# Kernel tuning notes

Hardware: AMD Instinct MI355X
Metric: run time of the kernel (lower is better)

## Reference

```python
import jax, jax.numpy as jnp
from jax import lax
import numpy as np

B, T, D, H = 64, 291, 300, 10
K = D // H  # 30
SLOPE = 0.01  # nn.LeakyReLU default
EPS = 1e-5


def _leaky(x):
    return jnp.where(x >= 0, x, SLOPE * x)


def _ln2d(x, g, b):
    # torch LayerNorm over the LAST TWO dims (normalized_shape=[t, d])
    mu = jnp.mean(x, axis=(-2, -1), keepdims=True)
    var = jnp.mean((x - mu) ** 2, axis=(-2, -1), keepdims=True)
    return (x - mu) / jnp.sqrt(var + EPS) * g + b


def _mha(x, Wq, Wk, Wv, Wm):
    # manual multi-head self-attention; q,k each scaled by h**-0.25
    b, t, d = x.shape
    s = H ** 0.25
    q = (x @ Wq.T).reshape(b, t, H, K) / s
    k = (x @ Wk.T).reshape(b, t, H, K) / s
    v = (x @ Wv.T).reshape(b, t, H, K)
    att = jax.nn.softmax(jnp.einsum('bihk,bjhk->bhij', q, k), axis=-1)
    o = jnp.einsum('bhij,bjhk->bihk', att, v).reshape(b, t, d)
    return o @ Wm.T


def _conv_head(R, W, b):
    # Conv2d(2,25,(kh,300)) valid -> [B,25,L,1]; leaky; global maxpool over L
    y = lax.conv_general_dilated(R, W, (1, 1), 'VALID',
                                 dimension_numbers=('NCHW', 'OIHW', 'NCHW'))
    y = _leaky(y + b[None, :, None, None])
    return jnp.max(y, axis=(2, 3))  # [B,25]


def setup_inputs() -> dict:
    key = jax.random.key(0)
    ks = jax.random.split(key, 32)
    it = iter(range(32))
    def n(shape, scale=0.05):
        return (jax.random.normal(ks[next(it)], shape, dtype=jnp.float32) * scale)
    inp = {
        'x1': jax.random.normal(ks[next(it)], (B, T, D), dtype=jnp.float32),
        'x2': jax.random.normal(ks[next(it)], (B, 1000), dtype=jnp.float32),
        'W_img': n((300, 1000)), 'b_img': jnp.zeros((300,), jnp.float32),
        'g1': jnp.ones((T, D), jnp.float32), 'be1': jnp.zeros((T, D), jnp.float32),
        'g2': jnp.ones((1, D), jnp.float32), 'be2': jnp.zeros((1, D), jnp.float32),
        'Wq_tp': n((D, D)), 'Wk_tp': n((D, D)), 'Wv_tp': n((D, D)),
        'Wq_pt': n((D, D)), 'Wk_pt': n((D, D)), 'Wv_pt': n((D, D)),
        'Wq1': n((D, D)), 'Wk1': n((D, D)), 'Wv1': n((D, D)), 'Wm1': n((D, D)),
        'Wq2': n((D, D)), 'Wk2': n((D, D)), 'Wv2': n((D, D)), 'Wm2': n((D, D)),
        'Wq3': n((D, D)), 'Wk3': n((D, D)), 'Wv3': n((D, D)), 'Wm3': n((D, D)),
        'Wc1': n((25, 2, 1, D)), 'Wc2': n((25, 2, 2, D)),
        'Wc3': n((25, 2, 3, D)), 'Wc4': n((25, 2, 4, D)),
        'bc1': jnp.zeros((25,), jnp.float32), 'bc2': jnp.zeros((25,), jnp.float32),
        'bc3': jnp.zeros((25,), jnp.float32), 'bc4': jnp.zeros((25,), jnp.float32),
        'Wlin': n((300, 100)), 'blin': jnp.zeros((300,), jnp.float32),
        'Wlast': n((2, 600)), 'blast': jnp.zeros((2,), jnp.float32),
    }
    return inp


def reference(x1, x2, W_img, b_img, g1, be1, g2, be2,
              Wq_tp, Wk_tp, Wv_tp, Wq_pt, Wk_pt, Wv_pt,
              Wq1, Wk1, Wv1, Wm1, Wq2, Wk2, Wv2, Wm2, Wq3, Wk3, Wv3, Wm3,
              Wc1, Wc2, Wc3, Wc4, bc1, bc2, bc3, bc4,
              Wlin, blin, Wlast, blast):
    # image branch: x2 is the frozen VGG19 1000-d encoding
    img = _leaky(x2 @ W_img.T + b_img)[:, None, :]      # [B,1,300]
    lnP = _ln2d(img, g2, be2)                           # [B,1,300]
    lnT = _ln2d(x1, g1, be1)                            # [B,291,300]

    # cross-attn T->P (query from image, kv from text), unscaled
    q = lnP @ Wq_tp.T; k = lnT @ Wk_tp.T; v = lnT @ Wv_tp.T
    a = jax.nn.softmax(jnp.einsum('bqd,btd->bqt', q, k), axis=-1)
    R_T_P = jnp.einsum('bqt,btd->bqd', a, v) + lnP      # [B,1,300]

    # cross-attn P->T (query from text, kv from image; softmax over size-1 dim)
    q = lnT @ Wq_pt.T; k = lnP @ Wk_pt.T; v = lnP @ Wv_pt.T
    a = jax.nn.softmax(jnp.einsum('btd,bqd->btq', q, k), axis=-1)
    R_P_T = jnp.einsum('btq,bqd->btd', a, v) + lnT      # [B,291,300]

    # 3 stacked multi-head self-attn blocks on the text stream
    a1 = _mha(lnT, Wq1, Wk1, Wv1, Wm1)
    a2 = _mha(a1, Wq2, Wk2, Wv2, Wm2)
    a3 = _mha(a2, Wq3, Wk3, Wv3, Wm3)

    R = jnp.stack((R_P_T, a3), axis=1)                  # [B,2,291,300]
    r1 = _conv_head(R, Wc1, bc1)
    r2 = _conv_head(R, Wc2, bc2)
    r3 = _conv_head(R, Wc3, bc3)
    r4 = _conv_head(R, Wc4, bc4)
    total = jnp.concatenate([r1, r2, r3, r4], axis=1)   # [B,100]
    total = _leaky(total @ Wlin.T + blin)               # [B,300]

    Y = jnp.concatenate([R_T_P[:, 0, :], total], axis=1) @ Wlast.T + blast
    return Y                                            # [B,2]
```

## Files before the change

kernel.cpp:

```cpp
#include <hip/hip_runtime.h>
#include <hip/hip_bf16.h>
#include <math.h>

#define Bn 64
#define Tn 291
#define Dn 300
#define Hn 10
#define Mn (Bn*Tn)
#define Mp 18688
#define Kp 320

typedef __bf16 bf16x8 __attribute__((ext_vector_type(8)));
typedef float f32x4 __attribute__((ext_vector_type(4)));

static __device__ __forceinline__ float leaky(float x){ return x >= 0.f ? x : 0.01f*x; }

template<int NT>
static __device__ __forceinline__ float blockSum(float v, float* red){
  __syncthreads();
  int lane = threadIdx.x & 63, wid = threadIdx.x >> 6;
  #pragma unroll
  for (int o = 32; o > 0; o >>= 1) v += __shfl_down(v, o, 64);
  if (lane == 0) red[wid] = v;
  __syncthreads();
  if (threadIdx.x == 0) {
    float s = red[0];
    #pragma unroll
    for (int w = 1; w < NT/64; ++w) s += red[w];
    red[0] = s;
  }
  __syncthreads();
  return red[0];
}

template<int NT>
static __device__ __forceinline__ float blockMax(float v, float* red){
  __syncthreads();
  int lane = threadIdx.x & 63, wid = threadIdx.x >> 6;
  #pragma unroll
  for (int o = 32; o > 0; o >>= 1) v = fmaxf(v, __shfl_down(v, o, 64));
  if (lane == 0) red[wid] = v;
  __syncthreads();
  if (threadIdx.x == 0) {
    float s = red[0];
    #pragma unroll
    for (int w = 1; w < NT/64; ++w) s = fmaxf(s, red[w]);
    red[0] = s;
  }
  __syncthreads();
  return red[0];
}

__global__ __launch_bounds__(256)
void k_img_lnp(const float* __restrict__ x2, const float* __restrict__ Wimg,
               const float* __restrict__ bimg, const float* __restrict__ g2,
               const float* __restrict__ be2, float* __restrict__ lnP)
{
  int b = blockIdx.x, tid = threadIdx.x;
  __shared__ float sx[1000];
  __shared__ float sy[300];
  __shared__ float red[4];
  for (int i = tid; i < 1000; i += 256) sx[i] = x2[b*1000 + i];
  __syncthreads();
  for (int j = tid; j < 300; j += 256) {
    const float* w = Wimg + j*1000;
    float a = 0.f;
    for (int i = 0; i < 1000; ++i) a += sx[i]*w[i];
    sy[j] = leaky(a + bimg[j]);
  }
  __syncthreads();
  float s = 0.f, ss = 0.f;
  for (int j = tid; j < 300; j += 256) { float v = sy[j]; s += v; ss += v*v; }
  float tot  = blockSum<256>(s, red);
  float tot2 = blockSum<256>(ss, red);
  float mu   = tot * (1.f/300.f);
  float var  = tot2 * (1.f/300.f) - mu*mu;
  float rstd = rsqrtf(var + 1e-5f);
  for (int j = tid; j < 300; j += 256)
    lnP[b*300 + j] = (sy[j]-mu)*rstd*g2[j] + be2[j];
}

__global__ __launch_bounds__(1024)
void k_lnT(const float* __restrict__ x1, const float* __restrict__ g1,
           const float* __restrict__ be1, float* __restrict__ outf,
           __hip_bfloat16* __restrict__ outb)
{
  int b = blockIdx.x, tid = threadIdx.x;
  __shared__ float red[16];
  const float4* xb = (const float4*)(x1 + (size_t)b*87300);
  const float4* g4 = (const float4*)g1;
  const float4* b4 = (const float4*)be1;
  float4* o4 = (float4*)(outf + (size_t)b*87300);
  float s = 0.f, ss = 0.f;
  for (int i = tid; i < 21825; i += 1024) {
    float4 v = xb[i];
    s  += v.x+v.y+v.z+v.w;
    ss += v.x*v.x+v.y*v.y+v.z*v.z+v.w*v.w;
  }
  float tot  = blockSum<1024>(s, red);
  float tot2 = blockSum<1024>(ss, red);
  float mu   = tot / 87300.f;
  float var  = tot2 / 87300.f - mu*mu;
  float rstd = rsqrtf(var + 1e-5f);
  for (int i = tid; i < 21825; i += 1024) {
    float4 v = xb[i], g = g4[i], be = b4[i], o;
    o.x = (v.x-mu)*rstd*g.x + be.x;
    o.y = (v.y-mu)*rstd*g.y + be.y;
    o.z = (v.z-mu)*rstd*g.z + be.z;
    o.w = (v.w-mu)*rstd*g.w + be.w;
    o4[i] = o;
  }
  const float* xs = x1 + (size_t)b*87300;
  for (int e = tid; e < Tn*Dn; e += 1024) {
    int t = e/300;
    float x = xs[e];
    outb[(size_t)(b*Tn+t)*Kp + (e - t*300)] = __float2bfloat16((x-mu)*rstd*g1[e] + be1[e]);
  }
  for (int e = tid; e < Tn*20; e += 1024) {
    int t = e/20, d = 300 + e%20;
    outb[(size_t)(b*Tn+t)*Kp + d] = __float2bfloat16(0.f);
  }
}

__global__ __launch_bounds__(320)
void k_tp(const float* __restrict__ lnP, const float* __restrict__ lnT,
          const float* __restrict__ Wq, const float* __restrict__ Wk,
          const float* __restrict__ Wv, const float* __restrict__ Wvpt,
          float* __restrict__ RTP, float* __restrict__ vpt)
{
  int b = blockIdx.x, tid = threadIdx.x;
  __shared__ float sP[300], sQ[300], sM[300], sA[291], sW[300], red[5];
  if (tid < 300) sP[tid] = lnP[b*300 + tid];
  __syncthreads();
  if (tid < 300) {
    const float* w = Wq + tid*300;
    float a = 0.f;
    for (int i = 0; i < 300; ++i) a += sP[i]*w[i];
    sQ[tid] = a;
  }
  __syncthreads();
  if (tid < 300) {
    float a = 0.f;
    for (int j = 0; j < 300; ++j) a += sQ[j]*Wk[j*300 + tid];
    sM[tid] = a;
  }
  __syncthreads();
  float sc = -1e30f;
  if (tid < 291) {
    const float* r = lnT + ((size_t)b*Tn + tid)*300;
    float a = 0.f;
    for (int i = 0; i < 300; ++i) a += r[i]*sM[i];
    sc = a;
  }
  float mx  = blockMax<320>(sc, red);
  float e   = (tid < 291) ? __expf(sc - mx) : 0.f;
  float den = blockSum<320>(e, red);
  if (tid < 291) sA[tid] = e;
  __syncthreads();
  if (tid < 300) {
    float a = 0.f;
    for (int t = 0; t < 291; ++t) a += sA[t]*lnT[((size_t)b*Tn + t)*300 + tid];
    sW[tid] = a / den;
  }
  __syncthreads();
  if (tid < 300) {
    const float* w = Wv + tid*300;
    float a = 0.f;
    for (int i = 0; i < 300; ++i) a += sW[i]*w[i];
    RTP[b*300 + tid] = a + sP[tid];
    const float* w2 = Wvpt + tid*300;
    float a2 = 0.f;
    for (int i = 0; i < 300; ++i) a2 += sP[i]*w2[i];
    vpt[b*300 + tid] = a2;
  }
}

__global__ __launch_bounds__(256)
void k_rptb(const float* __restrict__ lnT, const float* __restrict__ vpt,
            __hip_bfloat16* __restrict__ out)
{
  int idx = blockIdx.x*256 + threadIdx.x;
  if (idx >= Mn*Kp) return;
  int m = idx / Kp, d = idx - m*Kp;
  int b = m / Tn;
  float v = (d < 300) ? lnT[(size_t)m*300 + d] + vpt[b*300 + d] : 0.f;
  out[idx] = __float2bfloat16(v);
}

struct Wptrs { const float* p[12]; };
__global__ __launch_bounds__(256)
void k_wcvt(Wptrs wp, __hip_bfloat16* __restrict__ out)
{
  int idx = blockIdx.x*256 + threadIdx.x;
  if (idx >= 12*Kp*Kp) return;
  int mat = idx / (Kp*Kp);
  int rem = idx - mat*(Kp*Kp);
  int r = rem / Kp, c = rem - r*Kp;
  float v = (r < 300 && c < 300) ? wp.p[mat][r*300 + c] : 0.f;
  out[idx] = __float2bfloat16(v);
}

__global__ __launch_bounds__(256)
void k_wpackb(const float* __restrict__ Wc1, const float* __restrict__ Wc2,
              const float* __restrict__ Wc3, const float* __restrict__ Wc4,
              __hip_bfloat16* __restrict__ out)
{
  int idx = blockIdx.x*256 + threadIdx.x;
  if (idx >= 2*256*Kp) return;
  int c  = idx % Kp;
  int rc = idx / Kp;
  int ch = rc / 256;
  int r  = rc % 256;
  float v = 0.f;
  if (r < 250 && c < 300) {
    const float* W; int kh, ro;
    if      (r < 25)  { W = Wc1; kh = 1; ro = r;      }
    else if (r < 75)  { W = Wc2; kh = 2; ro = r - 25; }
    else if (r < 150) { W = Wc3; kh = 3; ro = r - 75; }
    else              { W = Wc4; kh = 4; ro = r - 150;}
    int o = ro/kh, dh = ro%kh;
    v = W[((o*2 + ch)*kh + dh)*300 + c];
  }
  out[idx] = __float2bfloat16(v);
}

__global__ __launch_bounds__(256)
void k_gemm3(const ushort* __restrict__ A0, const ushort* __restrict__ A1,
             const ushort* __restrict__ W0, const ushort* __restrict__ W1,
             ushort* __restrict__ C0, ushort* __restrict__ C1,
             int nn, int cpitch)
{
  const ushort* A = blockIdx.z ? A1 : A0;
  const ushort* W = blockIdx.z ? W1 : W0;
  ushort*       C = blockIdx.z ? C1 : C0;
  int total = gridDim.x;
  int bid = blockIdx.x;
  int q = total >> 3, r = total & 7;
  int xcd = bid & 7, idx = bid >> 3;
  int wgid = (xcd < r ? xcd*(q+1) : r*(q+1) + (xcd-r)*q) + idx;
  int m0 = (wgid / nn) * 128, n0 = (wgid % nn) * 64;

  __shared__ alignas(16) ushort As[2][128*64];
  __shared__ alignas(16) ushort Bs[2][64*64];
  int tid = threadIdx.x;
  int lane = tid & 63, w = tid >> 6, wr = w >> 1, wc = w & 1;
  int lm = lane & 15, lk = lane >> 4;
  f32x4 acc[4][2] = {};
  uint4 ra[4], rw[2];

  auto loadregs = [&](int kt){
    #pragma unroll
    for (int u = 0; u < 4; ++u) {
      int s = tid + u*256; int row = s >> 3, kg = s & 7;
      ra[u] = *(const uint4*)(A + (size_t)(m0+row)*Kp + kt*64 + kg*8);
    }
    #pragma unroll
    for (int u = 0; u < 2; ++u) {
      int s = tid + u*256; int row = s >> 3, kg = s & 7;
      rw[u] = *(const uint4*)(W + (size_t)(n0+row)*Kp + kt*64 + kg*8);
    }
  };
  auto writeLDS = [&](int buf){
    #pragma unroll
    for (int u = 0; u < 4; ++u) {
      int s = tid + u*256; int row = s >> 3, kg = s & 7;
      *(uint4*)&As[buf][row*64 + ((kg ^ (row&7)) << 3)] = ra[u];
    }
    #pragma unroll
    for (int u = 0; u < 2; ++u) {
      int s = tid + u*256; int row = s >> 3, kg = s & 7;
      *(uint4*)&Bs[buf][row*64 + ((kg ^ (row&7)) << 3)] = rw[u];
    }
  };
  auto compute = [&](int buf){
    #pragma unroll
    for (int s = 0; s < 2; ++s) {
      bf16x8 af[4], bfr[2];
      int kg = s*4 + lk;
      #pragma unroll
      for (int mf = 0; mf < 4; ++mf) {
        int rr = wr*64 + mf*16 + lm;
        af[mf] = *(const bf16x8*)&As[buf][rr*64 + ((kg ^ (rr&7)) << 3)];
      }
      #pragma unroll
      for (int nf = 0; nf < 2; ++nf) {
        int rr = wc*32 + nf*16 + lm;
        bfr[nf] = *(const bf16x8*)&Bs[buf][rr*64 + ((kg ^ (rr&7)) << 3)];
      }
      #pragma unroll
      for (int mf = 0; mf < 4; ++mf)
        #pragma unroll
        for (int nf = 0; nf < 2; ++nf)
          acc[mf][nf] = __builtin_amdgcn_mfma_f32_16x16x32_bf16(af[mf], bfr[nf], acc[mf][nf], 0, 0, 0);
    }
  };

  loadregs(0); writeLDS(0);
  __syncthreads();
  #pragma unroll 1
  for (int kt = 0; kt < 5; ++kt) {
    if (kt < 4) loadregs(kt+1);
    compute(kt & 1);
    if (kt < 4) {
      __syncthreads();
      writeLDS((kt+1) & 1);
      __syncthreads();
    }
  }
  __syncthreads();
  ushort* T = &As[0][0];
  #pragma unroll
  for (int mf = 0; mf < 4; ++mf)
    #pragma unroll
    for (int nf = 0; nf < 2; ++nf)
      #pragma unroll
      for (int i = 0; i < 4; ++i) {
        int rr = wr*64 + mf*16 + lk*4 + i;
        int cc = wc*32 + nf*16 + lm;
        __hip_bfloat16 t = __float2bfloat16(acc[mf][nf][i]);
        T[rr*72 + cc] = *(ushort*)&t;
      }
  __syncthreads();
  #pragma unroll
  for (int u = 0; u < 4; ++u) {
    int s = tid + u*256; int row = s >> 3, g = s & 7;
    uint4 v = *(const uint4*)&T[row*72 + g*8];
    *(uint4*)(C + (size_t)(m0+row)*cpitch + n0 + g*8) = v;
  }
}

__global__ __launch_bounds__(256)
void k_attn5(const ushort* __restrict__ X, ushort* __restrict__ O)
{
  int b = blockIdx.x, h = blockIdx.y, tid = threadIdx.x;
  __shared__ alignas(16) ushort Ks[320*40];
  __shared__ alignas(16) ushort Vt[32*328];
  __shared__ alignas(16) ushort Ps[64*168];
  const size_t rbase = (size_t)b*Tn*960;
  const int hq = h*30;
  for (int i = tid; i < 320*20; i += 256) {
    int r = i/20, c2 = i%20;
    uint v = 0u;
    if (r < Tn && c2 < 15) v = *(const uint*)(X + rbase + (size_t)r*960 + 320 + hq + 2*c2);
    *(uint*)&Ks[r*40 + 2*c2] = v;
  }
  for (int i = tid; i < 320*16; i += 256) {
    int j = i >> 4, c2 = i & 15;
    if (c2 < 15) {
      uint v = (j < Tn) ? *(const uint*)(X + rbase + (size_t)j*960 + 640 + hq + 2*c2) : 0u;
      Vt[(2*c2)*328 + j]   = (ushort)(v & 0xffffu);
      Vt[(2*c2+1)*328 + j] = (ushort)(v >> 16);
    } else {
      Vt[30*328 + j] = 0; Vt[31*328 + j] = 0;
    }
  }
  __syncthreads();
  int lane = tid & 63, w = tid >> 6;
  int lm = lane & 15, lk = lane >> 4;
  int qloc = w*16 + lm;
  const float scale = 0.31622776601683794f;
  #pragma unroll 1
  for (int qt = 0; qt < 5; ++qt) {
    int qrow = qt*64 + w*16 + lm;
    union { uint u[4]; bf16x8 v; } qq;
    {
      const uint* qp = (const uint*)(X + rbase + (size_t)qrow*960 + hq + lk*8);
      qq.u[0]=qp[0]; qq.u[1]=qp[1]; qq.u[2]=qp[2]; qq.u[3]=qp[3];
    }
    bf16x8 qf = qq.v;
    float rsum = 0.f;
    f32x4 oacc[2] = {};
    #pragma unroll 1
    for (int jh = 0; jh < 2; ++jh) {
      #pragma unroll
      for (int jtl = 0; jtl < 10; ++jtl) {
        int jt = jh*10 + jtl;
        bf16x8 kf = *(const bf16x8*)&Ks[(jt*16+lm)*40 + lk*8];
        f32x4 s = {};
        s = __builtin_amdgcn_mfma_f32_16x16x32_bf16(kf, qf, s, 0, 0, 0);
        union { ushort u[4]; uint2 v2; } pk;
        #pragma unroll
        for (int i2 = 0; i2 < 4; ++i2) {
          int j = jt*16 + lk*4 + i2;
          float p = (j < Tn) ? __expf(s[i2]*scale) : 0.f;
          rsum += p;
          __hip_bfloat16 t = __float2bfloat16(p);
          pk.u[i2] = *(ushort*)&t;
        }
        *(uint2*)&Ps[qloc*168 + jtl*16 + lk*4] = pk.v2;
      }
      #pragma unroll
      for (int ktl = 0; ktl < 5; ++ktl) {
        bf16x8 pf = *(const bf16x8*)&Ps[qloc*168 + ktl*32 + lk*8];
        int jb = jh*160 + ktl*32 + lk*8;
        #pragma unroll
        for (int nf = 0; nf < 2; ++nf) {
          bf16x8 vf = *(const bf16x8*)&Vt[(nf*16+lm)*328 + jb];
          oacc[nf] = __builtin_amdgcn_mfma_f32_16x16x32_bf16(pf, vf, oacc[nf], 0, 0, 0);
        }
      }
    }
    rsum += __shfl_xor(rsum, 16, 64);
    rsum += __shfl_xor(rsum, 32, 64);
    float inv[4];
    #pragma unroll
    for (int i2 = 0; i2 < 4; ++i2) inv[i2] = 1.f / __shfl(rsum, lk*4 + i2, 64);
    #pragma unroll
    for (int nf = 0; nf < 2; ++nf) {
      int d = nf*16 + lm;
      if (d < 30) {
        #pragma unroll
        for (int i2 = 0; i2 < 4; ++i2) {
          int qrw = qt*64 + w*16 + lk*4 + i2;
          if (qrw < Tn) {
            __hip_bfloat16 t = __float2bfloat16(oacc[nf][i2]*inv[i2]);
            O[((size_t)b*Tn + qrw)*Kp + hq + d] = *(ushort*)&t;
          }
        }
      }
    }
  }
}

__global__ __launch_bounds__(256)
void k_convred2(const ushort* __restrict__ G0, const ushort* __restrict__ G1,
                const float* __restrict__ bc1, const float* __restrict__ bc2,
                const float* __restrict__ bc3, const float* __restrict__ bc4,
                float* __restrict__ out100)
{
  int b = blockIdx.x, head = blockIdx.y;
  int kh  = head + 1;
  int off = (head == 0) ? 0 : (head == 1) ? 25 : (head == 2) ? 75 : 150;
  const float* bc = (head == 0) ? bc1 : (head == 1) ? bc2 : (head == 2) ? bc3 : bc4;
  int ncol = 25*kh;
  int ncp  = ncol | 1;
  int L = Tn - kh + 1;
  __shared__ float S[67*101];
  int tid = threadIdx.x, lane = tid & 63;
  float mx[7];
  #pragma unroll
  for (int u = 0; u < 7; ++u) mx[u] = -1e30f;
  for (int l0 = 0; l0 < L; l0 += 64) {
    int nrows = min(64 + kh - 1, Tn - l0);
    __syncthreads();
    for (int i = tid; i < nrows*ncol; i += 256) {
      int r = i / ncol, c = i % ncol;
      size_t g = (size_t)(b*Tn + l0 + r)*256 + off + c;
      __hip_bfloat16 a = *(const __hip_bfloat16*)&G0[g];
      __hip_bfloat16 d = *(const __hip_bfloat16*)&G1[g];
      S[r*ncp + c] = __bfloat162float(a) + __bfloat162float(d);
    }
    __syncthreads();
    int lmax = min(64, L - l0);
    #pragma unroll
    for (int u = 0; u < 7; ++u) {
      int o = (tid >> 6) + u*4;
      int dl = lane;
      if (o < 25 && dl < lmax) {
        float s = bc[o];
        for (int dh = 0; dh < kh; ++dh)
          s += S[(dl+dh)*ncp + o*kh + dh];
        mx[u] = fmaxf(mx[u], leaky(s));
      }
    }
  }
  #pragma unroll
  for (int u = 0; u < 7; ++u) {
    float v = mx[u];
    #pragma unroll
    for (int ofs = 32; ofs > 0; ofs >>= 1) v = fmaxf(v, __shfl_down(v, ofs, 64));
    int o = (tid >> 6) + u*4;
    if (lane == 0 && o < 25)
      out100[b*100 + head*25 + o] = v;
  }
}

__global__ __launch_bounds__(320)
void k_final(const float* __restrict__ RTP, const float* __restrict__ out100,
             const float* __restrict__ Wlin, const float* __restrict__ blin,
             const float* __restrict__ Wlast, const float* __restrict__ blast,
             float* __restrict__ Y)
{
  int b = blockIdx.x, tid = threadIdx.x;
  __shared__ float cat[600];
  __shared__ float s100[100];
  __shared__ float red[5];
  if (tid < 100) s100[tid] = out100[b*100 + tid];
  if (tid < 300) cat[tid] = RTP[b*300 + tid];
  __syncthreads();
  if (tid < 300) {
    const float* w = Wlin + tid*100;
    float a = blin[tid];
    for (int j = 0; j < 100; ++j) a += s100[j]*w[j];
    cat[300 + tid] = leaky(a);
  }
  __syncthreads();
  for (int c = 0; c < 2; ++c) {
    float a = 0.f;
    for (int i = tid; i < 600; i += 320) a += cat[i]*Wlast[c*600 + i];
    a = blockSum<320>(a, red);
    if (tid == 0) Y[b*2 + c] = a + blast[c];
  }
}

extern "C" void kernel_launch(void* const* d_in, const int* in_sizes, int n_in,
                              void* d_out, int out_size, void* d_ws, size_t ws_size,
                              hipStream_t stream)
{
  (void)in_sizes; (void)n_in; (void)out_size; (void)ws_size;
  const float* x1    = (const float*)d_in[0];
  const float* x2    = (const float*)d_in[1];
  const float* Wimg  = (const float*)d_in[2];
  const float* bimg  = (const float*)d_in[3];
  const float* g1    = (const float*)d_in[4];
  const float* be1   = (const float*)d_in[5];
  const float* g2    = (const float*)d_in[6];
  const float* be2   = (const float*)d_in[7];
  const float* Wq_tp = (const float*)d_in[8];
  const float* Wk_tp = (const float*)d_in[9];
  const float* Wv_tp = (const float*)d_in[10];
  const float* Wv_pt = (const float*)d_in[13];
  const float* Wc1 = (const float*)d_in[26];
  const float* Wc2 = (const float*)d_in[27];
  const float* Wc3 = (const float*)d_in[28];
  const float* Wc4 = (const float*)d_in[29];
  const float* bc1 = (const float*)d_in[30];
  const float* bc2 = (const float*)d_in[31];
  const float* bc3 = (const float*)d_in[32];
  const float* bc4 = (const float*)d_in[33];
  const float* Wlin  = (const float*)d_in[34];
  const float* blin  = (const float*)d_in[35];
  const float* Wlast = (const float*)d_in[36];
  const float* blast = (const float*)d_in[37];

  char* base = (char*)d_ws;
  float* lnP    = (float*)(base + 0);
  float* RTP    = (float*)(base + 76800);
  float* vpt    = (float*)(base + 153600);
  float* out100 = (float*)(base + 230400);
  float* lnTf   = (float*)(base + 262144);
  ushort* G0    = (ushort*)(base + 262144);
  ushort* G1    = (ushort*)(base + 262144 + 9568256);
  ushort* X960  = (ushort*)(base + 22610944);
  ushort* P0    = (ushort*)(base + 58491904);
  ushort* P1    = (ushort*)(base + 70452224);
  ushort* P2    = (ushort*)(base + 82412544);
  ushort* Wb    = (ushort*)(base + 94372864);
  ushort* Wpb   = (ushort*)(base + 96830464);
  const int WS = Kp*Kp;

  k_img_lnp<<<Bn, 256, 0, stream>>>(x2, Wimg, bimg, g2, be2, lnP);
  k_lnT<<<Bn, 1024, 0, stream>>>(x1, g1, be1, lnTf, (__hip_bfloat16*)P0);
  k_tp<<<Bn, 320, 0, stream>>>(lnP, lnTf, Wq_tp, Wk_tp, Wv_tp, Wv_pt, RTP, vpt);
  k_rptb<<<(Mn*Kp + 255)/256, 256, 0, stream>>>(lnTf, vpt, (__hip_bfloat16*)P1);

  Wptrs wp;
  for (int i = 0; i < 12; ++i) wp.p[i] = (const float*)d_in[14 + i];
  k_wcvt<<<(12*WS + 255)/256, 256, 0, stream>>>(wp, (__hip_bfloat16*)Wb);
  k_wpackb<<<(2*256*Kp + 255)/256, 256, 0, stream>>>(Wc1, Wc2, Wc3, Wc4, (__hip_bfloat16*)Wpb);

  dim3 gqkv(146*15, 1, 1), gproj(146*5, 1, 1), gconv(146*4, 1, 2), gat(Bn, Hn);
  for (int l = 0; l < 3; ++l) {
    const ushort* Wqkv = Wb + (size_t)l*4*WS;
    const ushort* Wm   = Wb + ((size_t)l*4+3)*WS;
    k_gemm3<<<gqkv, 256, 0, stream>>>(P0, P0, Wqkv, Wqkv, X960, X960, 15, 960);
    k_attn5<<<gat, 256, 0, stream>>>(X960, P2);
    k_gemm3<<<gproj, 256, 0, stream>>>(P2, P2, Wm, Wm, P0, P0, 5, 320);
  }
  k_gemm3<<<gconv, 256, 0, stream>>>(P1, P0, Wpb, Wpb + 256*Kp, G0, G1, 4, 256);
  k_convred2<<<dim3(Bn,4), 256, 0, stream>>>(G0, G1, bc1, bc2, bc3, bc4, out100);
  k_final<<<Bn, 320, 0, stream>>>(RTP, out100, Wlin, blin, Wlast, blast, (float*)d_out);
}
```

Measured before the change: 860.8 us.

## Store QKV projections in head-padded 64-column panels for aligned attention loads

The QKV weights are repacked so each head occupies 32 padded rows (1024 output columns in total). The QKV GEMM then writes its output in 64-column panel-major layout, so each attention block reads K, V and Q from contiguous 128-byte rows instead of strided 960-wide rows. This aims to make attention tile loads coalesced and drop the per-element bounds handling on the head dimension. In exchange the QKV GEMM does about 7% more work (16 column tiles instead of 15) and needs extra weight-repacking logic.

```diff
diff --git a/kernel.cpp b/kernel.cpp
--- a/kernel.cpp
+++ b/kernel.cpp
@@ -188,11 +188,29 @@
 }
 
 struct Wptrs { const float* p[12]; };
-__global__ __launch_bounds__(256)
-void k_wcvt(Wptrs wp, __hip_bfloat16* __restrict__ out)
+
+__global__ __launch_bounds__(256)
+void k_wqkv(Wptrs wp, __hip_bfloat16* __restrict__ out)
 {
   int idx = blockIdx.x*256 + threadIdx.x;
-  if (idx >= 12*Kp*Kp) return;
+  if (idx >= 3*1024*Kp) return;
+  int l = idx / (1024*Kp);
+  int rem = idx - l*(1024*Kp);
+  int rowp = rem / Kp, c = rem - rowp*Kp;
+  int hh = rowp >> 5, j = rowp & 31;
+  float v = 0.f;
+  if (j < 30 && c < 300 && hh < 30) {
+    int g = hh/10;
+    v = wp.p[l*3 + g][((hh - g*10)*30 + j)*300 + c];
+  }
+  out[idx] = __float2bfloat16(v);
+}
+
+__global__ __launch_bounds__(256)
+void k_wcvt(Wptrs wp, __hip_bfloat16* __restrict__ out, int nmat)
+{
+  int idx = blockIdx.x*256 + threadIdx.x;
+  if (idx >= nmat*Kp*Kp) return;
   int mat = idx / (Kp*Kp);
   int rem = idx - mat*(Kp*Kp);
   int r = rem / Kp, c = rem - r*Kp;
@@ -224,6 +242,7 @@
   out[idx] = __float2bfloat16(v);
 }
 
+template<bool PANEL>
 __global__ __launch_bounds__(256)
 void k_gemm3(const ushort* __restrict__ A0, const ushort* __restrict__ A1,
              const ushort* __restrict__ W0, const ushort* __restrict__ W1,
@@ -325,34 +344,33 @@
   for (int u = 0; u < 4; ++u) {
     int s = tid + u*256; int row = s >> 3, g = s & 7;
     uint4 v = *(const uint4*)&T[row*72 + g*8];
-    *(uint4*)(C + (size_t)(m0+row)*cpitch + n0 + g*8) = v;
-  }
-}
-
-__global__ __launch_bounds__(256)
-void k_attn5(const ushort* __restrict__ X, ushort* __restrict__ O)
+    if (PANEL)
+      *(uint4*)(C + ((size_t)(n0 >> 6)*Mp + m0 + row)*64 + g*8) = v;
+    else
+      *(uint4*)(C + (size_t)(m0+row)*cpitch + n0 + g*8) = v;
+  }
+}
+
+__global__ __launch_bounds__(256)
+void k_attn6(const ushort* __restrict__ Xp, ushort* __restrict__ O)
 {
   int b = blockIdx.x, h = blockIdx.y, tid = threadIdx.x;
   __shared__ alignas(16) ushort Ks[320*40];
   __shared__ alignas(16) ushort Vt[32*328];
   __shared__ alignas(16) ushort Ps[64*168];
-  const size_t rbase = (size_t)b*Tn*960;
+  const size_t rb = (size_t)b*Tn;
+  const int Pq = h >> 1, off = (h & 1)*32;
   const int hq = h*30;
-  for (int i = tid; i < 320*20; i += 256) {
-    int r = i/20, c2 = i%20;
-    uint v = 0u;
-    if (r < Tn && c2 < 15) v = *(const uint*)(X + rbase + (size_t)r*960 + 320 + hq + 2*c2);
+  for (int i = tid; i < 320*16; i += 256) {
+    int r = i >> 4, c2 = i & 15;
+    uint v = (r < Tn) ? *(const uint*)(Xp + ((size_t)(5+Pq)*Mp + rb + r)*64 + off + 2*c2) : 0u;
     *(uint*)&Ks[r*40 + 2*c2] = v;
   }
   for (int i = tid; i < 320*16; i += 256) {
     int j = i >> 4, c2 = i & 15;
-    if (c2 < 15) {
-      uint v = (j < Tn) ? *(const uint*)(X + rbase + (size_t)j*960 + 640 + hq + 2*c2) : 0u;
-      Vt[(2*c2)*328 + j]   = (ushort)(v & 0xffffu);
-      Vt[(2*c2+1)*328 + j] = (ushort)(v >> 16);
-    } else {
-      Vt[30*328 + j] = 0; Vt[31*328 + j] = 0;
-    }
+    uint v = (j < Tn) ? *(const uint*)(Xp + ((size_t)(10+Pq)*Mp + rb + j)*64 + off + 2*c2) : 0u;
+    Vt[(2*c2)*328 + j]   = (ushort)(v & 0xffffu);
+    Vt[(2*c2+1)*328 + j] = (ushort)(v >> 16);
   }
   __syncthreads();
   int lane = tid & 63, w = tid >> 6;
@@ -364,7 +382,7 @@
     int qrow = qt*64 + w*16 + lm;
     union { uint u[4]; bf16x8 v; } qq;
     {
-      const uint* qp = (const uint*)(X + rbase + (size_t)qrow*960 + hq + lk*8);
+      const uint* qp = (const uint*)(Xp + ((size_t)Pq*Mp + rb + qrow)*64 + off + lk*8);
       qq.u[0]=qp[0]; qq.u[1]=qp[1]; qq.u[2]=qp[2]; qq.u[3]=qp[3];
     }
     bf16x8 qf = qq.v;
@@ -414,7 +432,7 @@
           int qrw = qt*64 + w*16 + lk*4 + i2;
           if (qrw < Tn) {
             __hip_bfloat16 t = __float2bfloat16(oacc[nf][i2]*inv[i2]);
-            O[((size_t)b*Tn + qrw)*Kp + hq + d] = *(ushort*)&t;
+            O[(rb + qrw)*Kp + hq + d] = *(ushort*)&t;
           }
         }
       }
@@ -538,15 +556,16 @@
   float* RTP    = (float*)(base + 76800);
   float* vpt    = (float*)(base + 153600);
   float* out100 = (float*)(base + 230400);
-  float* lnTf   = (float*)(base + 262144);
+  float*  lnTf  = (float*)(base + 262144);
+  ushort* X1024 = (ushort*)(base + 262144);
   ushort* G0    = (ushort*)(base + 262144);
   ushort* G1    = (ushort*)(base + 262144 + 9568256);
-  ushort* X960  = (ushort*)(base + 22610944);
-  ushort* P0    = (ushort*)(base + 58491904);
-  ushort* P1    = (ushort*)(base + 70452224);
-  ushort* P2    = (ushort*)(base + 82412544);
-  ushort* Wb    = (ushort*)(base + 94372864);
-  ushort* Wpb   = (ushort*)(base + 96830464);
+  ushort* P0    = (ushort*)(base + 38535168);
+  ushort* P1    = (ushort*)(base + 50495488);
+  ushort* P2    = (ushort*)(base + 62455808);
+  ushort* Wpad  = (ushort*)(base + 74416128);
+  ushort* Wm    = (ushort*)(base + 76382208);
+  ushort* Wpb   = (ushort*)(base + 76996608);
   const int WS = Kp*Kp;
 
   k_img_lnp<<<Bn, 256, 0, stream>>>(x2, Wimg, bimg, g2, be2, lnP);
@@ -554,20 +573,25 @@
   k_tp<<<Bn, 320, 0, stream>>>(lnP, lnTf, Wq_tp, Wk_tp, Wv_tp, Wv_pt, RTP, vpt);
   k_rptb<<<(Mn*Kp + 255)/256, 256, 0, stream>>>(lnTf, vpt, (__hip_bfloat16*)P1);
 
-  Wptrs wp;
-  for (int i = 0; i < 12; ++i) wp.p[i] = (const float*)d_in[14 + i];
-  k_wcvt<<<(12*WS + 255)/256, 256, 0, stream>>>(wp, (__hip_bfloat16*)Wb);
+  Wptrs wq;
+  wq.p[0]=(const float*)d_in[14]; wq.p[1]=(const float*)d_in[15]; wq.p[2]=(const float*)d_in[16];
+  wq.p[3]=(const float*)d_in[18]; wq.p[4]=(const float*)d_in[19]; wq.p[5]=(const float*)d_in[20];
+  wq.p[6]=(const float*)d_in[22]; wq.p[7]=(const float*)d_in[23]; wq.p[8]=(const float*)d_in[24];
+  k_wqkv<<<(3*1024*Kp + 255)/256, 256, 0, stream>>>(wq, (__hip_bfloat16*)Wpad);
+  Wptrs wm;
+  wm.p[0]=(const float*)d_in[17]; wm.p[1]=(const float*)d_in[21]; wm.p[2]=(const float*)d_in[25];
+  k_wcvt<<<(3*WS + 255)/256, 256, 0, stream>>>(wm, (__hip_bfloat16*)Wm, 3);
   k_wpackb<<<(2*256*Kp + 255)/256, 256, 0, stream>>>(Wc1, Wc2, Wc3, Wc4, (__hip_bfloat16*)Wpb);
 
-  dim3 gqkv(146*15, 1, 1), gproj(146*5, 1, 1), gconv(146*4, 1, 2), gat(Bn, Hn);
+  dim3 gqkv(146*16, 1, 1), gproj(146*5, 1, 1), gconv(146*4, 1, 2), gat(Bn, Hn);
   for (int l = 0; l < 3; ++l) {
-    const ushort* Wqkv = Wb + (size_t)l*4*WS;
-    const ushort* Wm   = Wb + ((size_t)l*4+3)*WS;
-    k_gemm3<<<gqkv, 256, 0, stream>>>(P0, P0, Wqkv, Wqkv, X960, X960, 15, 960);
-    k_attn5<<<gat, 256, 0, stream>>>(X960, P2);
-    k_gemm3<<<gproj, 256, 0, stream>>>(P2, P2, Wm, Wm, P0, P0, 5, 320);
-  }
-  k_gemm3<<<gconv, 256, 0, stream>>>(P1, P0, Wpb, Wpb + 256*Kp, G0, G1, 4, 256);
+    const ushort* Wq3 = Wpad + (size_t)l*1024*Kp;
+    const ushort* Wm3 = Wm + (size_t)l*WS;
+    k_gemm3<true ><<<gqkv, 256, 0, stream>>>(P0, P0, Wq3, Wq3, X1024, X1024, 16, 0);
+    k_attn6<<<gat, 256, 0, stream>>>(X1024, P2);
+    k_gemm3<false><<<gproj, 256, 0, stream>>>(P2, P2, Wm3, Wm3, P0, P0, 5, 320);
+  }
+  k_gemm3<false><<<gconv, 256, 0, stream>>>(P1, P0, Wpb, Wpb + 256*Kp, G0, G1, 4, 256);
   k_convred2<<<dim3(Bn,4), 256, 0, stream>>>(G0, G1, bc1, bc2, bc3, bc4, out100);
   k_final<<<Bn, 320, 0, stream>>>(RTP, out100, Wlin, blin, Wlast, blast, (float*)d_out);
 }
```

Result: no change. 853.0 us (-0.9%).
